# Optimization experiments

Measured on AMD Instinct MI355X. Metric: run time of the kernel, lower is better.

## Reference

```python
import jax, jax.numpy as jnp
import numpy as np

N_HEAD = 4
GROUPS = 32
EPS = 1e-5


def group_norm(x, scale, bias):
    B, C, H, W = x.shape
    xg = x.reshape(B, GROUPS, C // GROUPS, H, W)
    mu = xg.mean(axis=(2, 3, 4), keepdims=True)
    var = xg.var(axis=(2, 3, 4), keepdims=True)
    xg = (xg - mu) * jax.lax.rsqrt(var + EPS)
    x = xg.reshape(B, C, H, W)
    return x * scale[None, :, None, None] + bias[None, :, None, None]


def setup_inputs() -> dict:
    key = jax.random.key(0)
    k0, k1, k2 = jax.random.split(key, 3)
    B, C, H, W = 2, 64, 64, 64
    x = jax.random.normal(k0, (B, C, H, W), dtype=jnp.float32)
    gn_scale = jnp.ones((C,), dtype=jnp.float32)
    gn_bias = jnp.zeros((C,), dtype=jnp.float32)
    w_qkv = jax.random.normal(k1, (3 * C, C), dtype=jnp.float32) * 0.05  # 1x1 conv, no bias
    w_out = jax.random.normal(k2, (C, C), dtype=jnp.float32) * 0.05     # 1x1 conv
    b_out = jnp.zeros((C,), dtype=jnp.float32)
    return {"x": x, "gn_scale": gn_scale, "gn_bias": gn_bias,
            "w_qkv": w_qkv, "w_out": w_out, "b_out": b_out}


def reference(x, gn_scale, gn_bias, w_qkv, w_out, b_out):
    B, C, H, W = x.shape
    head_dim = C // N_HEAD
    norm = group_norm(x, gn_scale, gn_bias)
    # 1x1 conv == channel matmul
    qkv = jnp.einsum('oc,bchw->bohw', w_qkv, norm)
    qkv = qkv.reshape(B, N_HEAD, head_dim * 3, H, W)
    q, k, v = jnp.split(qkv, 3, axis=2)  # each [B, n, head_dim, H, W]
    # full spatial attention scores, scaled by sqrt(channel) as in source
    attn = jnp.einsum('bnchw,bncyx->bnhwyx', q, k) / jnp.sqrt(jnp.float32(C))
    attn = jax.nn.softmax(attn.reshape(B, N_HEAD, H, W, H * W), axis=-1)
    attn = attn.reshape(B, N_HEAD, H, W, H, W)
    out = jnp.einsum('bnhwyx,bncyx->bnchw', attn, v).reshape(B, C, H, W)
    out = jnp.einsum('oc,bchw->bohw', w_out, out) + b_out[None, :, None, None]
    return out + x
```

## Files before the change

### kernel.cpp

```cpp
#include <hip/hip_runtime.h>
#include <hip/hip_bf16.h>

typedef __attribute__((ext_vector_type(8))) short short8;
typedef __attribute__((ext_vector_type(4))) float f32x4;
typedef __attribute__((ext_vector_type(16))) float f32x16;
typedef __attribute__((ext_vector_type(4))) unsigned int uint4v;
typedef __attribute__((ext_vector_type(4))) unsigned short ushort4v;

#define DEV static __device__ __forceinline__

DEV unsigned short f2bf(float f){
  unsigned u = __float_as_uint(f);
  u += 0x7fffu + ((u >> 16) & 1u);
  return (unsigned short)(u >> 16);
}

DEV float bf2f(unsigned short h){
  unsigned u = ((unsigned)h) << 16;
  float f;
  __builtin_memcpy(&f, &u, 4);
  return f;
}

DEV unsigned pack2bf(float a, float b){
  __hip_bfloat162 h = __float22bfloat162_rn(make_float2(a, b));
  unsigned u;
  __builtin_memcpy(&u, &h, 4);
  return u;
}

#define QSCALE 0.180336880111f
#define NSPLIT 8
#define NT 8

__global__ __launch_bounds__(256) void gn_partial_k(const float* __restrict__ x,
                                                    float* __restrict__ gp){
  int blk = blockIdx.x;
  float4 v = ((const float4*)(x + (size_t)blk*1024))[threadIdx.x];
  float s = v.x+v.y+v.z+v.w;
  float q = v.x*v.x+v.y*v.y+v.z*v.z+v.w*v.w;
  #pragma unroll
  for (int off = 1; off < 64; off <<= 1){
    s += __shfl_xor(s, off);
    q += __shfl_xor(q, off);
  }
  __shared__ float red[8];
  int w = threadIdx.x >> 6;
  if ((threadIdx.x & 63) == 0){ red[w*2] = s; red[w*2+1] = q; }
  __syncthreads();
  if (threadIdx.x == 0){
    gp[blk*2+0] = red[0]+red[2]+red[4]+red[6];
    gp[blk*2+1] = red[1]+red[3]+red[5]+red[7];
  }
}

__global__ __launch_bounds__(256) void qkv_k(const float* __restrict__ x,
    const float* __restrict__ gp, const float* __restrict__ gsc,
    const float* __restrict__ gbi, const float* __restrict__ wq,
    unsigned short* __restrict__ q, unsigned short* __restrict__ k,
    unsigned short* __restrict__ vt){
  int b  = blockIdx.x >> 8;
  int s0 = (blockIdx.x & 255) * 16;
  __shared__ float W[192][68];
  __shared__ float A[16][68];
  __shared__ float MS[32][2];
  int t = threadIdx.x;
  for (int i = t; i < 3072; i += 256){
    int o = i >> 4, c4 = (i & 15) * 4;
    *(float4*)&W[o][c4] = ((const float4*)wq)[i];
  }
  if (t < 32){
    float s = 0.f, ss = 0.f;
    #pragma unroll
    for (int i = 0; i < 8; ++i){
      const float* pp = gp + ((b*32 + t)*8 + i)*2;
      s += pp[0]; ss += pp[1];
    }
    float mean = s * (1.f/8192.f);
    MS[t][0] = mean;
    MS[t][1] = rsqrtf(ss * (1.f/8192.f) - mean*mean + 1e-5f);
  }
  __syncthreads();
  {
    int c  = t >> 2;
    int s4 = (t & 3) * 4;
    const float* px = x + ((size_t)b*64 + c)*4096 + s0 + s4;
    float4 v0 = *(const float4*)px;
    float sc = gsc[c] * MS[c>>1][1];
    float bi = gbi[c] - MS[c>>1][0] * sc;
    A[s4+0][c]=v0.x*sc+bi; A[s4+1][c]=v0.y*sc+bi;
    A[s4+2][c]=v0.z*sc+bi; A[s4+3][c]=v0.w*sc+bi;
  }
  __syncthreads();
  int sl = t >> 4, grp = t & 15;
  float acc[12];
  #pragma unroll
  for (int j = 0; j < 12; ++j) acc[j] = 0.f;
  for (int c4 = 0; c4 < 16; ++c4){
    float4 a = *(const float4*)&A[sl][c4*4];
    #pragma unroll
    for (int j = 0; j < 12; ++j){
      float4 wv = *(const float4*)&W[grp + j*16][c4*4];
      acc[j] = fmaf(a.x, wv.x, fmaf(a.y, wv.y, fmaf(a.z, wv.z, fmaf(a.w, wv.w, acc[j]))));
    }
  }
  int s = s0 + sl;
  int slp = (sl & 0x3) | (((sl >> 2) & 1) << 3) | (((sl >> 3) & 1) << 2);
  #pragma unroll
  for (int j = 0; j < 12; ++j){
    int o = grp + j*16;
    int n = o / 48, r = o % 48;
    float val = acc[j];
    if (r < 16){
      q[(((size_t)b*4 + n)*4096 + s)*16 + r] = f2bf(val * QSCALE);
    } else if (r < 32){
      k[(((size_t)b*4 + n)*4096 + s)*16 + r - 16] = f2bf(val);
    } else {
      vt[((size_t)(b*4 + n)*16 + (r - 32))*4096 + s0 + slp] = f2bf(val);
    }
  }
}

__global__ __launch_bounds__(256, 5) void attn_k(const unsigned short* __restrict__ qb,
    const unsigned short* __restrict__ kb, const unsigned short* __restrict__ vt,
    unsigned short* __restrict__ part, float* __restrict__ lsums){
  int blk = blockIdx.x;
  int bn = blk & 7;
  int sp = (blk >> 3) & (NSPLIT - 1);
  int qg = blk >> 6;
  int t = threadIdx.x, w = t >> 6, l = t & 63;
  int lq = l & 31, hi = l >> 5;

  __shared__ unsigned short Klds[8192];

  {
    const unsigned short* ksrc = kb + ((size_t)bn*4096 + sp*512)*16;
    #pragma unroll
    for (int p = 0; p < 4; ++p){
      int G = p*256 + t;
      *(short8*)&Klds[G*8] = *(const short8*)(ksrc + (size_t)G*8);
    }
  }

  int qrow = qg*128 + w*32;
  short8 qf = *(const short8*)(qb + ((size_t)bn*4096 + qrow)*16 + (size_t)lq*16 + hi*8);

  const unsigned short* vaddr = vt + ((size_t)bn*16 + (lq & 15))*4096 + sp*512 + hi*8;
  bool vld = (lq < 16);

  short8 vsel;
  {
    unsigned short c = (lq == 16) ? (unsigned short)0x3F80 : (unsigned short)0;
    #pragma unroll
    for (int r = 0; r < 8; ++r) vsel[r] = (short)c;
  }

  f32x16 O, zero;
  #pragma unroll
  for (int r = 0; r < 16; ++r){ O[r] = 0.f; zero[r] = 0.f; }

  __syncthreads();

  short8 kf0 = *(const short8*)&Klds[(size_t)lq*16 + hi*8];
  short8 kf1 = *(const short8*)&Klds[(size_t)(32 + lq)*16 + hi*8];

  #pragma unroll 1
  for (int kt = 0; kt < NT; ++kt){
    short8 v0 = vsel, v1 = vsel, v2 = vsel, v3 = vsel;
    if (vld){
      const unsigned short* va = vaddr + (size_t)kt*64;
      v0 = *(const short8*)(va);
      v1 = *(const short8*)(va + 16);
      v2 = *(const short8*)(va + 32);
      v3 = *(const short8*)(va + 48);
    }
    short8 kn0 = {}, kn1 = {};
    if (kt + 1 < NT){
      kn0 = *(const short8*)&Klds[(size_t)((kt+1)*64 + lq)*16 + hi*8];
      kn1 = *(const short8*)&Klds[(size_t)((kt+1)*64 + 32 + lq)*16 + hi*8];
    }

    __builtin_amdgcn_s_setprio(1);
    f32x16 sA = __builtin_amdgcn_mfma_f32_32x32x16_bf16(kf0, qf, zero, 0, 0, 0);
    f32x16 sB = __builtin_amdgcn_mfma_f32_32x32x16_bf16(kf1, qf, zero, 0, 0, 0);
    __builtin_amdgcn_s_setprio(0);

    #pragma unroll
    for (int r = 0; r < 16; ++r) sA[r] = __builtin_amdgcn_exp2f(sA[r]);
    #pragma unroll
    for (int r = 0; r < 16; ++r) sB[r] = __builtin_amdgcn_exp2f(sB[r]);

    auto pvstep = [&](const f32x16& pc, int h8, short8 vf){
      uint4v pw;
      pw[0] = pack2bf(pc[h8+0], pc[h8+1]);
      pw[1] = pack2bf(pc[h8+2], pc[h8+3]);
      pw[2] = pack2bf(pc[h8+4], pc[h8+5]);
      pw[3] = pack2bf(pc[h8+6], pc[h8+7]);
      short8 pa = __builtin_bit_cast(short8, pw);
      O = __builtin_amdgcn_mfma_f32_32x32x16_bf16(pa, vf, O, 0, 0, 0);
    };
    __builtin_amdgcn_s_setprio(1);
    pvstep(sA, 0, v0);
    pvstep(sA, 8, v1);
    pvstep(sB, 0, v2);
    pvstep(sB, 8, v3);
    __builtin_amdgcn_s_setprio(0);

    kf0 = kn0; kf1 = kn1;
  }

  unsigned short* Op = part + (((size_t)sp*8 + bn)*4096 + qrow)*16;
  size_t lbase = ((size_t)sp*8 + bn)*4096 + qrow;
  #pragma unroll
  for (int r = 0; r < 16; ++r){
    int qr = (r&3) + 8*(r>>2) + 4*hi;
    if (lq < 16) __builtin_nontemporal_store(f2bf(O[r]), &Op[(size_t)qr*16 + lq]);
  }
  if (lq == 16){
    #pragma unroll
    for (int r = 0; r < 16; ++r){
      int qr = (r&3) + 8*(r>>2) + 4*hi;
      __builtin_nontemporal_store(O[r], &lsums[lbase + qr]);
    }
  }
}

__global__ __launch_bounds__(256) void oproj_k(const unsigned short* __restrict__ part,
    const float* __restrict__ lsums, const float* __restrict__ wo,
    const float* __restrict__ bo, const float* __restrict__ x,
    float* __restrict__ out){
  int b  = blockIdx.x >> 8;
  int s0 = (blockIdx.x & 255) * 16;
  __shared__ float W[64][68];
  __shared__ float A[16][68];
  int t = threadIdx.x;
  for (int i = t; i < 1024; i += 256){
    int o = i >> 4, c4 = (i & 15) * 4;
    *(float4*)&W[o][c4] = ((const float4*)wo)[i];
  }
  {
    int sl = t & 15;
    int u  = t >> 4;
    int n = u >> 2, d4 = (u & 3) * 4;
    size_t row = ((size_t)b*4 + n)*4096 + s0 + sl;
    float L = 0.f;
    #pragma unroll
    for (int sp = 0; sp < NSPLIT; ++sp)
      L += __builtin_nontemporal_load(&lsums[(size_t)sp*32768 + row]);
    f32x4 acc = {0.f,0.f,0.f,0.f};
    #pragma unroll
    for (int sp = 0; sp < NSPLIT; ++sp){
      ushort4v u0 = *(const ushort4v*)(part + ((size_t)sp*32768 + row)*16 + d4);
      acc[0] += bf2f(u0[0]); acc[1] += bf2f(u0[1]);
      acc[2] += bf2f(u0[2]); acc[3] += bf2f(u0[3]);
    }
    float inv = 1.f / L;
    A[sl][n*16+d4+0] = acc[0]*inv; A[sl][n*16+d4+1] = acc[1]*inv;
    A[sl][n*16+d4+2] = acc[2]*inv; A[sl][n*16+d4+3] = acc[3]*inv;
  }
  __syncthreads();
  int sl = t & 15, grp = t >> 4;
  float acc[4] = {0.f,0.f,0.f,0.f};
  for (int c4 = 0; c4 < 16; ++c4){
    float4 a = *(const float4*)&A[sl][c4*4];
    #pragma unroll
    for (int j = 0; j < 4; ++j){
      float4 wv = *(const float4*)&W[grp + j*16][c4*4];
      acc[j] = fmaf(a.x, wv.x, fmaf(a.y, wv.y, fmaf(a.z, wv.z, fmaf(a.w, wv.w, acc[j]))));
    }
  }
  int s = s0 + sl;
  #pragma unroll
  for (int j = 0; j < 4; ++j){
    int o = grp + j*16;
    size_t idx = ((size_t)b*64 + o)*4096 + s;
    out[idx] = acc[j] + bo[o] + x[idx];
  }
}

extern "C" void kernel_launch(void* const* d_in, const int* in_sizes, int n_in,
                              void* d_out, int out_size, void* d_ws, size_t ws_size,
                              hipStream_t stream){
  const float* x   = (const float*)d_in[0];
  const float* gsc = (const float*)d_in[1];
  const float* gbi = (const float*)d_in[2];
  const float* wq  = (const float*)d_in[3];
  const float* wo  = (const float*)d_in[4];
  const float* bo  = (const float*)d_in[5];
  float* out = (float*)d_out;

  char* ws = (char*)d_ws;
  float* gp           = (float*)ws;
  unsigned short* q   = (unsigned short*)(ws + 8192);
  unsigned short* k   = (unsigned short*)(ws + 8192 + 1048576);
  unsigned short* vt  = (unsigned short*)(ws + 8192 + 2097152);
  unsigned short* part= (unsigned short*)(ws + 8192 + 3145728);
  float* lsums        = (float*)(ws + 8192 + 3145728 + 8388608);

  gn_partial_k<<<512,  256, 0, stream>>>(x, gp);
  qkv_k       <<<512,  256, 0, stream>>>(x, gp, gsc, gbi, wq, q, k, vt);
  attn_k      <<<2048, 256, 0, stream>>>(q, k, vt, part, lsums);
  oproj_k     <<<512,  256, 0, stream>>>(part, lsums, wo, bo, x, out);
}
```

Before: 55.56 us.

## Software-pipeline QK and PV MFMAs across iterations with dual accumulators

Restructures the attention inner loop so the QK score MFMAs for the next key tile are issued alongside the PV MFMAs for the current tile. The exp2 and bf16 packing then overlap with matrix work instead of serialising after it. The output accumulator is split into two independent chains (O0/O1) to shorten MFMA dependency chains, and the two are summed at the end. This raises register pressure, so the launch-bounds occupancy hint is lowered from 5 to 4 waves.

```diff
diff --git a/kernel.cpp b/kernel.cpp
--- a/kernel.cpp
+++ b/kernel.cpp
@@ -121,7 +121,7 @@
   }
 }
 
-__global__ __launch_bounds__(256, 5) void attn_k(const unsigned short* __restrict__ qb,
+__global__ __launch_bounds__(256, 4) void attn_k(const unsigned short* __restrict__ qb,
     const unsigned short* __restrict__ kb, const unsigned short* __restrict__ vt,
     unsigned short* __restrict__ part, float* __restrict__ lsums){
   int blk = blockIdx.x;
@@ -155,72 +155,92 @@
     for (int r = 0; r < 8; ++r) vsel[r] = (short)c;
   }
 
-  f32x16 O, zero;
-  #pragma unroll
-  for (int r = 0; r < 16; ++r){ O[r] = 0.f; zero[r] = 0.f; }
-
-  __syncthreads();
+  f32x16 O0, O1, zero;
+  #pragma unroll
+  for (int r = 0; r < 16; ++r){ O0[r] = 0.f; O1[r] = 0.f; zero[r] = 0.f; }
+
+  __syncthreads();
+
+  auto packP = [&](const f32x16& pc, int h8) -> short8 {
+    uint4v pw;
+    pw[0] = pack2bf(pc[h8+0], pc[h8+1]);
+    pw[1] = pack2bf(pc[h8+2], pc[h8+3]);
+    pw[2] = pack2bf(pc[h8+4], pc[h8+5]);
+    pw[3] = pack2bf(pc[h8+6], pc[h8+7]);
+    return __builtin_bit_cast(short8, pw);
+  };
 
   short8 kf0 = *(const short8*)&Klds[(size_t)lq*16 + hi*8];
   short8 kf1 = *(const short8*)&Klds[(size_t)(32 + lq)*16 + hi*8];
+  f32x16 sA = __builtin_amdgcn_mfma_f32_32x32x16_bf16(kf0, qf, zero, 0, 0, 0);
+  f32x16 sB = __builtin_amdgcn_mfma_f32_32x32x16_bf16(kf1, qf, zero, 0, 0, 0);
+  kf0 = *(const short8*)&Klds[(size_t)(64 + lq)*16 + hi*8];
+  kf1 = *(const short8*)&Klds[(size_t)(96 + lq)*16 + hi*8];
+  short8 v0 = vsel, v1 = vsel, v2 = vsel, v3 = vsel;
+  if (vld){
+    v0 = *(const short8*)(vaddr);
+    v1 = *(const short8*)(vaddr + 16);
+    v2 = *(const short8*)(vaddr + 32);
+    v3 = *(const short8*)(vaddr + 48);
+  }
+  #pragma unroll
+  for (int r = 0; r < 16; ++r) sA[r] = __builtin_amdgcn_exp2f(sA[r]);
+  #pragma unroll
+  for (int r = 0; r < 16; ++r) sB[r] = __builtin_amdgcn_exp2f(sB[r]);
+  short8 paA0 = packP(sA, 0), paA1 = packP(sA, 8);
+  short8 paB0 = packP(sB, 0), paB1 = packP(sB, 8);
 
   #pragma unroll 1
-  for (int kt = 0; kt < NT; ++kt){
-    short8 v0 = vsel, v1 = vsel, v2 = vsel, v3 = vsel;
+  for (int kt = 0; kt < NT-1; ++kt){
+    __builtin_amdgcn_s_setprio(1);
+    f32x16 nA = __builtin_amdgcn_mfma_f32_32x32x16_bf16(kf0, qf, zero, 0, 0, 0);
+    f32x16 nB = __builtin_amdgcn_mfma_f32_32x32x16_bf16(kf1, qf, zero, 0, 0, 0);
+    O0 = __builtin_amdgcn_mfma_f32_32x32x16_bf16(paA0, v0, O0, 0, 0, 0);
+    O1 = __builtin_amdgcn_mfma_f32_32x32x16_bf16(paA1, v1, O1, 0, 0, 0);
+    O0 = __builtin_amdgcn_mfma_f32_32x32x16_bf16(paB0, v2, O0, 0, 0, 0);
+    O1 = __builtin_amdgcn_mfma_f32_32x32x16_bf16(paB1, v3, O1, 0, 0, 0);
+    __builtin_amdgcn_s_setprio(0);
+    if (kt + 2 < NT){
+      kf0 = *(const short8*)&Klds[(size_t)((kt+2)*64 + lq)*16 + hi*8];
+      kf1 = *(const short8*)&Klds[(size_t)((kt+2)*64 + 32 + lq)*16 + hi*8];
+    }
+    v0 = vsel; v1 = vsel; v2 = vsel; v3 = vsel;
     if (vld){
-      const unsigned short* va = vaddr + (size_t)kt*64;
+      const unsigned short* va = vaddr + (size_t)(kt+1)*64;
       v0 = *(const short8*)(va);
       v1 = *(const short8*)(va + 16);
       v2 = *(const short8*)(va + 32);
       v3 = *(const short8*)(va + 48);
     }
-    short8 kn0 = {}, kn1 = {};
-    if (kt + 1 < NT){
-      kn0 = *(const short8*)&Klds[(size_t)((kt+1)*64 + lq)*16 + hi*8];
-      kn1 = *(const short8*)&Klds[(size_t)((kt+1)*64 + 32 + lq)*16 + hi*8];
-    }
-
-    __builtin_amdgcn_s_setprio(1);
-    f32x16 sA = __builtin_amdgcn_mfma_f32_32x32x16_bf16(kf0, qf, zero, 0, 0, 0);
-    f32x16 sB = __builtin_amdgcn_mfma_f32_32x32x16_bf16(kf1, qf, zero, 0, 0, 0);
-    __builtin_amdgcn_s_setprio(0);
-
-    #pragma unroll
-    for (int r = 0; r < 16; ++r) sA[r] = __builtin_amdgcn_exp2f(sA[r]);
-    #pragma unroll
-    for (int r = 0; r < 16; ++r) sB[r] = __builtin_amdgcn_exp2f(sB[r]);
-
-    auto pvstep = [&](const f32x16& pc, int h8, short8 vf){
-      uint4v pw;
-      pw[0] = pack2bf(pc[h8+0], pc[h8+1]);
-      pw[1] = pack2bf(pc[h8+2], pc[h8+3]);
-      pw[2] = pack2bf(pc[h8+4], pc[h8+5]);
-      pw[3] = pack2bf(pc[h8+6], pc[h8+7]);
-      short8 pa = __builtin_bit_cast(short8, pw);
-      O = __builtin_amdgcn_mfma_f32_32x32x16_bf16(pa, vf, O, 0, 0, 0);
-    };
-    __builtin_amdgcn_s_setprio(1);
-    pvstep(sA, 0, v0);
-    pvstep(sA, 8, v1);
-    pvstep(sB, 0, v2);
-    pvstep(sB, 8, v3);
-    __builtin_amdgcn_s_setprio(0);
-
-    kf0 = kn0; kf1 = kn1;
-  }
+    #pragma unroll
+    for (int r = 0; r < 16; ++r) nA[r] = __builtin_amdgcn_exp2f(nA[r]);
+    #pragma unroll
+    for (int r = 0; r < 16; ++r) nB[r] = __builtin_amdgcn_exp2f(nB[r]);
+    paA0 = packP(nA, 0); paA1 = packP(nA, 8);
+    paB0 = packP(nB, 0); paB1 = packP(nB, 8);
+  }
+
+  __builtin_amdgcn_s_setprio(1);
+  O0 = __builtin_amdgcn_mfma_f32_32x32x16_bf16(paA0, v0, O0, 0, 0, 0);
+  O1 = __builtin_amdgcn_mfma_f32_32x32x16_bf16(paA1, v1, O1, 0, 0, 0);
+  O0 = __builtin_amdgcn_mfma_f32_32x32x16_bf16(paB0, v2, O0, 0, 0, 0);
+  O1 = __builtin_amdgcn_mfma_f32_32x32x16_bf16(paB1, v3, O1, 0, 0, 0);
+  __builtin_amdgcn_s_setprio(0);
+  #pragma unroll
+  for (int r = 0; r < 16; ++r) O0[r] += O1[r];
 
   unsigned short* Op = part + (((size_t)sp*8 + bn)*4096 + qrow)*16;
   size_t lbase = ((size_t)sp*8 + bn)*4096 + qrow;
   #pragma unroll
   for (int r = 0; r < 16; ++r){
     int qr = (r&3) + 8*(r>>2) + 4*hi;
-    if (lq < 16) __builtin_nontemporal_store(f2bf(O[r]), &Op[(size_t)qr*16 + lq]);
+    if (lq < 16) __builtin_nontemporal_store(f2bf(O0[r]), &Op[(size_t)qr*16 + lq]);
   }
   if (lq == 16){
     #pragma unroll
     for (int r = 0; r < 16; ++r){
       int qr = (r&3) + 8*(r>>2) + 4*hi;
-      __builtin_nontemporal_store(O[r], &lsums[lbase + qr]);
+      __builtin_nontemporal_store(O0[r], &lsums[lbase + qr]);
     }
   }
 }
```

Measured after the change: 55.60 us. No clear change (+0.1%).
